# Kernel optimization log

Hardware: AMD Instinct MI355X
Metric: run time of the kernel (lower is better)

Reference implementation:

```python
import jax, jax.numpy as jnp
import numpy as np

BETA = 10.0  # fixed buffer: torch.ones(1, num_centers) * 10


def setup_inputs() -> dict:
    key = jax.random.key(0)
    k1, k2, k3 = jax.random.split(key, 3)
    n, M, d, n_out = 65536, 1024, 64, 3
    x = jax.random.normal(k1, (n, d), dtype=jnp.float32)
    centers = jax.random.normal(k2, (M, d), dtype=jnp.float32)
    # nn.Linear init in the module: weight ~ N(0, 0.02), bias = 0
    W = jax.random.normal(k3, (n_out, M + d), dtype=jnp.float32) * 0.02
    b = jnp.zeros((n_out,), dtype=jnp.float32)
    return {"x": x, "centers": centers, "W": W, "b": b}


def reference(x, centers, W, b):
    x2 = jnp.sum(x * x, axis=1, keepdims=True)          # [n, 1]
    c2 = jnp.sum(centers * centers, axis=1)             # [M]
    d2 = x2 + c2[None, :] - 2.0 * (x @ centers.T)       # [n, M]
    rbf = jnp.exp(-BETA * d2)                           # Gaussian RBF
    feat = jnp.concatenate([x, rbf], axis=1)            # [n, d + M]
    return feat @ W.T + b                               # [n, n_out]
```

## Files before the change

kernel.cpp:

```cpp
#include <hip/hip_runtime.h>
#include <math.h>

typedef short bf16x8 __attribute__((ext_vector_type(8)));
typedef float f32x4 __attribute__((ext_vector_type(4)));
typedef unsigned int uint32;

#define BETA 10.0f
#define THRESH -80.0f

#define C_OFF    0
#define C2_OFF   131072
#define XB_OFF   135168
#define W_OFF    151552
#define X2_OFF   152320
#define RED_OFF  152832
#define LDS_TOT  155904

__device__ __forceinline__ uint32 f2bf_rtne(float f) {
    uint32 u = __float_as_uint(f);
    u += 0x7FFFu + ((u >> 16) & 1u);
    return u >> 16;
}
__device__ __forceinline__ uint32 pk_rtne(float a, float b) {
    return f2bf_rtne(a) | (f2bf_rtne(b) << 16);
}
__device__ __forceinline__ float bf2f(short s) {
    return __uint_as_float(((uint32)(unsigned short)s) << 16);
}
__device__ __forceinline__ f32x4 vmax4(f32x4 a, f32x4 b) {
    f32x4 r;
    r[0] = fmaxf(a[0], b[0]); r[1] = fmaxf(a[1], b[1]);
    r[2] = fmaxf(a[2], b[2]); r[3] = fmaxf(a[3], b[3]);
    return r;
}

#define GLDS(g, l) __builtin_amdgcn_global_load_lds( \
    (const __attribute__((address_space(1))) unsigned int*)(g), \
    (__attribute__((address_space(3))) unsigned int*)(l), 16, 0, 0)

__global__ void rbfn_prep(const float* __restrict__ centers,
                          uint32* __restrict__ cbf,
                          float* __restrict__ c2m) {
    const int tid = threadIdx.x;
    const int j = blockIdx.x * 64 + (tid >> 2);
    const int seg = tid & 3;
    const float4* cp = (const float4*)(centers + j * 64 + seg * 16);
    const float4 f0 = cp[0], f1 = cp[1], f2 = cp[2], f3 = cp[3];
    float s = f0.x*f0.x + f0.y*f0.y + f0.z*f0.z + f0.w*f0.w
            + f1.x*f1.x + f1.y*f1.y + f1.z*f1.z + f1.w*f1.w
            + f2.x*f2.x + f2.y*f2.y + f2.z*f2.z + f2.w*f2.w
            + f3.x*f3.x + f3.y*f3.y + f3.z*f3.z + f3.w*f3.w;
    uint4 p0, p1;
    p0.x = pk_rtne(f0.x, f0.y); p0.y = pk_rtne(f0.z, f0.w);
    p0.z = pk_rtne(f1.x, f1.y); p0.w = pk_rtne(f1.z, f1.w);
    p1.x = pk_rtne(f2.x, f2.y); p1.y = pk_rtne(f2.z, f2.w);
    p1.z = pk_rtne(f3.x, f3.y); p1.w = pk_rtne(f3.z, f3.w);
    char* base = (char*)cbf + (j >> 4) * 2048 + (j & 15) * 16;
    *(uint4*)(base + (seg * 2 + 0) * 256) = p0;
    *(uint4*)(base + (seg * 2 + 1) * 256) = p1;
    s += __shfl_xor(s, 1);
    s += __shfl_xor(s, 2);
    if (seg == 0) c2m[j] = -BETA * s;
}

__global__ __launch_bounds__(512, 2) void rbfn_main(
    const float* __restrict__ x,
    const char* __restrict__ ws,
    const float* __restrict__ W,
    const float* __restrict__ bias,
    const float* __restrict__ centers,
    float* __restrict__ out)
{
    __shared__ __align__(16) char lds[LDS_TOT];

    const int tid = threadIdx.x;
    const int wv = tid >> 6;
    const int lane = tid & 63;
    const int quad = lane >> 4;
    const int l15 = lane & 15;
    const int row0 = blockIdx.x * 256;

    const float bb0 = bias[0], bb1 = bias[1], bb2 = bias[2];

    {
        const char* g = ws + wv * 1024 + lane * 16;
        char* l = lds + wv * 1024;
        #pragma unroll
        for (int it = 0; it < 16; ++it)
            GLDS(g + it * 8192, l + it * 8192);
        if (wv < 4)
            GLDS(ws + 131072 + wv * 1024 + lane * 16, lds + 131072 + wv * 1024);
    }

    float4 xv[2][4];
    {
        const float4* xg = (const float4*)(x + (size_t)row0 * 64);
        #pragma unroll
        for (int i = 0; i < 4; ++i) xv[0][i] = xg[tid + 512 * i];
        #pragma unroll
        for (int i = 0; i < 4; ++i) xv[1][i] = xg[2048 + tid + 512 * i];
    }
    if (tid < 48) {
        const int k = tid >> 4, c = tid & 15;
        *((float4*)(lds + W_OFF) + tid) = *((const float4*)(W + k * 1088) + c);
    }
    #pragma unroll
    for (int i = 0; i < 4; ++i) {
        const int f = tid + 512 * i;
        const float4 v = xv[0][i];
        const int row = f >> 4, sg = f & 15;
        uint2 q; q.x = pk_rtne(v.x, v.y); q.y = pk_rtne(v.z, v.w);
        *(uint2*)(lds + XB_OFF + (row >> 4) * 2048 + (sg >> 1) * 256 +
                  (row & 15) * 16 + (sg & 1) * 8) = q;
    }

    __syncthreads();

    bf16x8 af[8][2];
    const char* cB = lds + wv * 16384 + quad * 256 + l15 * 16;
    const float* c2p = (const float*)(lds + C2_OFF) + wv * 128 + l15;

    #pragma unroll
    for (int t = 0; t < 2; ++t) {
        #pragma unroll
        for (int rt = 0; rt < 8; ++rt) {
            const char* ab = lds + XB_OFF + rt * 2048 + l15 * 16;
            af[rt][0] = *(const bf16x8*)(ab + quad * 256);
            af[rt][1] = *(const bf16x8*)(ab + (4 + quad) * 256);
        }
        {
            const int r = tid >> 2, qq = tid & 3;
            const char* xr = lds + XB_OFF + (r >> 4) * 2048 + (r & 15) * 16;
            const bf16x8 h0 = *(const bf16x8*)(xr + (qq * 2 + 0) * 256);
            const bf16x8 h1 = *(const bf16x8*)(xr + (qq * 2 + 1) * 256);
            const float* w0 = (const float*)(lds + W_OFF) + 0 * 64 + qq * 16;
            const float* w1 = (const float*)(lds + W_OFF) + 1 * 64 + qq * 16;
            const float* w2 = (const float*)(lds + W_OFF) + 2 * 64 + qq * 16;
            float s2 = 0.f, d0 = 0.f, d1 = 0.f, d2 = 0.f;
            #pragma unroll
            for (int e = 0; e < 8; ++e) {
                const float a = bf2f(h0[e]), b = bf2f(h1[e]);
                s2 = fmaf(a, a, s2); s2 = fmaf(b, b, s2);
                d0 = fmaf(a, w0[e], d0); d0 = fmaf(b, w0[8 + e], d0);
                d1 = fmaf(a, w1[e], d1); d1 = fmaf(b, w1[8 + e], d1);
                d2 = fmaf(a, w2[e], d2); d2 = fmaf(b, w2[8 + e], d2);
            }
            #pragma unroll
            for (int m = 1; m <= 2; m <<= 1) {
                s2 += __shfl_xor(s2, m);
                d0 += __shfl_xor(d0, m);
                d1 += __shfl_xor(d1, m);
                d2 += __shfl_xor(d2, m);
            }
            if (qq == 0) {
                ((float*)(lds + X2_OFF))[r] = s2;
                float* red = (float*)(lds + RED_OFF + t * 1536);
                red[r * 3 + 0] = d0 + bb0;
                red[r * 3 + 1] = d1 + bb1;
                red[r * 3 + 2] = d2 + bb2;
            }
        }
        __syncthreads();

        if (t == 0) {
            #pragma unroll
            for (int i = 0; i < 4; ++i) {
                const int f = tid + 512 * i;
                const float4 v = xv[1][i];
                const int row = f >> 4, sg = f & 15;
                uint2 q; q.x = pk_rtne(v.x, v.y); q.y = pk_rtne(v.z, v.w);
                *(uint2*)(lds + XB_OFF + (row >> 4) * 2048 + (sg >> 1) * 256 +
                          (row & 15) * 16 + (sg & 1) * 8) = q;
            }
        }

        const float* px2 = (const float*)(lds + X2_OFF);
        float mn = 1e30f;
        #pragma unroll
        for (int rt = 0; rt < 8; ++rt) {
            const float4 q4 = *(const float4*)(px2 + rt * 16 + quad * 4);
            mn = fminf(mn, fminf(fminf(q4.x, q4.y), fminf(q4.z, q4.w)));
        }
        const float prermax = -BETA * mn;

        float gm = -1e30f;
        #pragma unroll
        for (int ct = 0; ct < 8; ++ct) {
            const bf16x8 b0 = *(const bf16x8*)(cB + ct * 2048);
            const bf16x8 b1 = *(const bf16x8*)(cB + ct * 2048 + 1024);
            const float c2v = c2p[ct * 16];
            f32x4 acc[8];
            #pragma unroll
            for (int rt = 0; rt < 8; ++rt) {
                const f32x4 z = {0.f, 0.f, 0.f, 0.f};
                acc[rt] = __builtin_amdgcn_mfma_f32_16x16x32_bf16(af[rt][0], b0, z, 0, 0, 0);
                acc[rt] = __builtin_amdgcn_mfma_f32_16x16x32_bf16(af[rt][1], b1, acc[rt], 0, 0, 0);
            }
            f32x4 m0 = vmax4(vmax4(acc[0], acc[1]), vmax4(acc[2], acc[3]));
            f32x4 m1 = vmax4(vmax4(acc[4], acc[5]), vmax4(acc[6], acc[7]));
            m0 = vmax4(m0, m1);
            const float m = fmaxf(fmaxf(m0[0], m0[1]), fmaxf(m0[2], m0[3]));
            gm = fmaxf(gm, fmaf(2.0f * BETA, m, c2v));
        }
        const float bound = gm + prermax;

        if (__builtin_expect(__ballot(bound > THRESH) != 0ull, 0)) {
            float* red = (float*)(lds + RED_OFF + t * 1536);
            #pragma clang loop unroll(disable)
            for (int ct = 0; ct < 8; ++ct) {
                const int j = wv * 128 + ct * 16 + l15;
                #pragma clang loop unroll(disable)
                for (int rr = 0; rr < 32; ++rr) {
                    const int r = (rr >> 2) * 16 + quad * 4 + (rr & 3);
                    const float* xr = x + (size_t)(row0 + t * 128 + r) * 64;
                    const float* cr = centers + (size_t)j * 64;
                    float d2 = 0.f;
                    #pragma clang loop unroll(disable)
                    for (int k = 0; k < 64; ++k) {
                        const float df = xr[k] - cr[k];
                        d2 = fmaf(df, df, d2);
                    }
                    const float arg = -BETA * d2;
                    if (arg > -87.f) {
                        const float e = expf(arg);
                        atomicAdd(&red[r * 3 + 0], e * W[0 * 1088 + 64 + j]);
                        atomicAdd(&red[r * 3 + 1], e * W[1 * 1088 + 64 + j]);
                        atomicAdd(&red[r * 3 + 2], e * W[2 * 1088 + 64 + j]);
                    }
                }
            }
        }
        __syncthreads();

        if (tid < 96)
            ((float4*)out)[blockIdx.x * 192 + t * 96 + tid] =
                *((const float4*)(lds + RED_OFF + t * 1536) + tid);
    }
}

extern "C" void kernel_launch(void* const* d_in, const int* in_sizes, int n_in,
                              void* d_out, int out_size, void* d_ws, size_t ws_size,
                              hipStream_t stream) {
    const float* x       = (const float*)d_in[0];
    const float* centers = (const float*)d_in[1];
    const float* W       = (const float*)d_in[2];
    const float* b       = (const float*)d_in[3];
    float* out = (float*)d_out;

    uint32* cbf = (uint32*)d_ws;
    float*  c2m = (float*)((char*)d_ws + 131072);

    const int n = in_sizes[0] / 64;

    rbfn_prep<<<16, 256, 0, stream>>>(centers, cbf, c2m);
    rbfn_main<<<n / 256, 512, 0, stream>>>(x, (const char*)d_ws, W, b, centers, out);
}
```

Before: 79.32 us.

## Split block work across 16 waves by row and column groups

Doubles the block to 1024 threads and splits the work: each wave now handles half the rows (rowgrp) of a 128-column slab (colgrp), so per-wave MFMA and register work halves. The x-norm and bias dot products are computed with 8 threads per row instead of 4, and the x2 buffer is double-buffered per tile. c2 values are hoisted into registers. The aim is more waves per CU to hide LDS and MFMA latency. In exchange the A fragments are loaded by more waves, and with about 153KB of LDS per block only one block fits per CU.

```diff
diff --git a/kernel.cpp b/kernel.cpp
--- a/kernel.cpp
+++ b/kernel.cpp
@@ -13,8 +13,8 @@
 #define XB_OFF   135168
 #define W_OFF    151552
 #define X2_OFF   152320
-#define RED_OFF  152832
-#define LDS_TOT  155904
+#define RED_OFF  153344
+#define LDS_TOT  156416
 
 __device__ __forceinline__ uint32 f2bf_rtne(float f) {
     uint32 u = __float_as_uint(f);
@@ -63,7 +63,7 @@
     if (seg == 0) c2m[j] = -BETA * s;
 }
 
-__global__ __launch_bounds__(512, 2) void rbfn_main(
+__global__ __launch_bounds__(1024) void rbfn_main(
     const float* __restrict__ x,
     const char* __restrict__ ws,
     const float* __restrict__ W,
@@ -78,35 +78,38 @@
     const int lane = tid & 63;
     const int quad = lane >> 4;
     const int l15 = lane & 15;
+    const int rowgrp = wv & 1;
+    const int colgrp = wv >> 1;
     const int row0 = blockIdx.x * 256;
 
     const float bb0 = bias[0], bb1 = bias[1], bb2 = bias[2];
 
     {
-        const char* g = ws + wv * 1024 + lane * 16;
-        char* l = lds + wv * 1024;
-        #pragma unroll
-        for (int it = 0; it < 16; ++it)
-            GLDS(g + it * 8192, l + it * 8192);
+        const char* g = ws + wv * 8192 + lane * 16;
+        char* l = lds + wv * 8192;
+        #pragma unroll
+        for (int it = 0; it < 8; ++it)
+            GLDS(g + it * 1024, l + it * 1024);
         if (wv < 4)
-            GLDS(ws + 131072 + wv * 1024 + lane * 16, lds + 131072 + wv * 1024);
-    }
-
-    float4 xv[2][4];
+            GLDS(ws + 131072 + wv * 1024 + lane * 16, lds + C2_OFF + wv * 1024);
+    }
+
+    float4 xv[2][2];
     {
         const float4* xg = (const float4*)(x + (size_t)row0 * 64);
         #pragma unroll
-        for (int i = 0; i < 4; ++i) xv[0][i] = xg[tid + 512 * i];
-        #pragma unroll
-        for (int i = 0; i < 4; ++i) xv[1][i] = xg[2048 + tid + 512 * i];
+        for (int t = 0; t < 2; ++t)
+            #pragma unroll
+            for (int i = 0; i < 2; ++i)
+                xv[t][i] = xg[t * 2048 + i * 1024 + tid];
     }
     if (tid < 48) {
         const int k = tid >> 4, c = tid & 15;
         *((float4*)(lds + W_OFF) + tid) = *((const float4*)(W + k * 1088) + c);
     }
     #pragma unroll
-    for (int i = 0; i < 4; ++i) {
-        const int f = tid + 512 * i;
+    for (int i = 0; i < 2; ++i) {
+        const int f = i * 1024 + tid;
         const float4 v = xv[0][i];
         const int row = f >> 4, sg = f & 15;
         uint2 q; q.x = pk_rtne(v.x, v.y); q.y = pk_rtne(v.z, v.w);
@@ -116,44 +119,48 @@
 
     __syncthreads();
 
-    bf16x8 af[8][2];
-    const char* cB = lds + wv * 16384 + quad * 256 + l15 * 16;
-    const float* c2p = (const float*)(lds + C2_OFF) + wv * 128 + l15;
+    float c2r[8];
+    {
+        const float* c2p = (const float*)(lds + C2_OFF) + colgrp * 128 + l15;
+        #pragma unroll
+        for (int ct = 0; ct < 8; ++ct) c2r[ct] = c2p[ct * 16];
+    }
+    const char* cB = lds + C_OFF + colgrp * 16384 + quad * 256 + l15 * 16;
 
     #pragma unroll
     for (int t = 0; t < 2; ++t) {
-        #pragma unroll
-        for (int rt = 0; rt < 8; ++rt) {
-            const char* ab = lds + XB_OFF + rt * 2048 + l15 * 16;
+        bf16x8 af[4][2];
+        #pragma unroll
+        for (int rt = 0; rt < 4; ++rt) {
+            const char* ab = lds + XB_OFF + (rowgrp * 4 + rt) * 2048 + l15 * 16;
             af[rt][0] = *(const bf16x8*)(ab + quad * 256);
             af[rt][1] = *(const bf16x8*)(ab + (4 + quad) * 256);
         }
         {
-            const int r = tid >> 2, qq = tid & 3;
-            const char* xr = lds + XB_OFF + (r >> 4) * 2048 + (r & 15) * 16;
-            const bf16x8 h0 = *(const bf16x8*)(xr + (qq * 2 + 0) * 256);
-            const bf16x8 h1 = *(const bf16x8*)(xr + (qq * 2 + 1) * 256);
-            const float* w0 = (const float*)(lds + W_OFF) + 0 * 64 + qq * 16;
-            const float* w1 = (const float*)(lds + W_OFF) + 1 * 64 + qq * 16;
-            const float* w2 = (const float*)(lds + W_OFF) + 2 * 64 + qq * 16;
+            const int r = tid >> 3, e = tid & 7;
+            const bf16x8 h = *(const bf16x8*)(lds + XB_OFF + (r >> 4) * 2048 +
+                                              e * 256 + (r & 15) * 16);
+            const float* w0 = (const float*)(lds + W_OFF) + 0 * 64 + e * 8;
+            const float* w1 = (const float*)(lds + W_OFF) + 1 * 64 + e * 8;
+            const float* w2 = (const float*)(lds + W_OFF) + 2 * 64 + e * 8;
             float s2 = 0.f, d0 = 0.f, d1 = 0.f, d2 = 0.f;
             #pragma unroll
-            for (int e = 0; e < 8; ++e) {
-                const float a = bf2f(h0[e]), b = bf2f(h1[e]);
-                s2 = fmaf(a, a, s2); s2 = fmaf(b, b, s2);
-                d0 = fmaf(a, w0[e], d0); d0 = fmaf(b, w0[8 + e], d0);
-                d1 = fmaf(a, w1[e], d1); d1 = fmaf(b, w1[8 + e], d1);
-                d2 = fmaf(a, w2[e], d2); d2 = fmaf(b, w2[8 + e], d2);
-            }
-            #pragma unroll
-            for (int m = 1; m <= 2; m <<= 1) {
+            for (int i = 0; i < 8; ++i) {
+                const float a = bf2f(h[i]);
+                s2 = fmaf(a, a, s2);
+                d0 = fmaf(a, w0[i], d0);
+                d1 = fmaf(a, w1[i], d1);
+                d2 = fmaf(a, w2[i], d2);
+            }
+            #pragma unroll
+            for (int m = 1; m <= 4; m <<= 1) {
                 s2 += __shfl_xor(s2, m);
                 d0 += __shfl_xor(d0, m);
                 d1 += __shfl_xor(d1, m);
                 d2 += __shfl_xor(d2, m);
             }
-            if (qq == 0) {
-                ((float*)(lds + X2_OFF))[r] = s2;
+            if (e == 0) {
+                ((float*)(lds + X2_OFF + t * 512))[r] = s2;
                 float* red = (float*)(lds + RED_OFF + t * 1536);
                 red[r * 3 + 0] = d0 + bb0;
                 red[r * 3 + 1] = d1 + bb1;
@@ -164,8 +171,8 @@
 
         if (t == 0) {
             #pragma unroll
-            for (int i = 0; i < 4; ++i) {
-                const int f = tid + 512 * i;
+            for (int i = 0; i < 2; ++i) {
+                const int f = i * 1024 + tid;
                 const float4 v = xv[1][i];
                 const int row = f >> 4, sg = f & 15;
                 uint2 q; q.x = pk_rtne(v.x, v.y); q.y = pk_rtne(v.z, v.w);
@@ -174,10 +181,10 @@
             }
         }
 
-        const float* px2 = (const float*)(lds + X2_OFF);
+        const float* px2 = (const float*)(lds + X2_OFF + t * 512) + rowgrp * 64;
         float mn = 1e30f;
         #pragma unroll
-        for (int rt = 0; rt < 8; ++rt) {
+        for (int rt = 0; rt < 4; ++rt) {
             const float4 q4 = *(const float4*)(px2 + rt * 16 + quad * 4);
             mn = fminf(mn, fminf(fminf(q4.x, q4.y), fminf(q4.z, q4.w)));
         }
@@ -188,19 +195,16 @@
         for (int ct = 0; ct < 8; ++ct) {
             const bf16x8 b0 = *(const bf16x8*)(cB + ct * 2048);
             const bf16x8 b1 = *(const bf16x8*)(cB + ct * 2048 + 1024);
-            const float c2v = c2p[ct * 16];
-            f32x4 acc[8];
-            #pragma unroll
-            for (int rt = 0; rt < 8; ++rt) {
+            f32x4 acc[4];
+            #pragma unroll
+            for (int rt = 0; rt < 4; ++rt) {
                 const f32x4 z = {0.f, 0.f, 0.f, 0.f};
                 acc[rt] = __builtin_amdgcn_mfma_f32_16x16x32_bf16(af[rt][0], b0, z, 0, 0, 0);
                 acc[rt] = __builtin_amdgcn_mfma_f32_16x16x32_bf16(af[rt][1], b1, acc[rt], 0, 0, 0);
             }
             f32x4 m0 = vmax4(vmax4(acc[0], acc[1]), vmax4(acc[2], acc[3]));
-            f32x4 m1 = vmax4(vmax4(acc[4], acc[5]), vmax4(acc[6], acc[7]));
-            m0 = vmax4(m0, m1);
             const float m = fmaxf(fmaxf(m0[0], m0[1]), fmaxf(m0[2], m0[3]));
-            gm = fmaxf(gm, fmaf(2.0f * BETA, m, c2v));
+            gm = fmaxf(gm, fmaf(2.0f * BETA, m, c2r[ct]));
         }
         const float bound = gm + prermax;
 
@@ -208,10 +212,10 @@
             float* red = (float*)(lds + RED_OFF + t * 1536);
             #pragma clang loop unroll(disable)
             for (int ct = 0; ct < 8; ++ct) {
-                const int j = wv * 128 + ct * 16 + l15;
+                const int j = colgrp * 128 + ct * 16 + l15;
                 #pragma clang loop unroll(disable)
-                for (int rr = 0; rr < 32; ++rr) {
-                    const int r = (rr >> 2) * 16 + quad * 4 + (rr & 3);
+                for (int rr = 0; rr < 16; ++rr) {
+                    const int r = rowgrp * 64 + (rr >> 2) * 16 + quad * 4 + (rr & 3);
                     const float* xr = x + (size_t)(row0 + t * 128 + r) * 64;
                     const float* cr = centers + (size_t)j * 64;
                     float d2 = 0.f;
@@ -253,5 +257,5 @@
     const int n = in_sizes[0] / 64;
 
     rbfn_prep<<<16, 256, 0, stream>>>(centers, cbf, c2m);
-    rbfn_main<<<n / 256, 512, 0, stream>>>(x, (const char*)d_ws, W, b, centers, out);
-}
+    rbfn_main<<<n / 256, 1024, 0, stream>>>(x, (const char*)d_ws, W, b, centers, out);
+}
```

New measurement: 81.53 us. +2.8%, slower.

## Fuse center prep into main kernel and compute norms and linear head via MFMA

Applied to the files above, without the earlier changes.

Removes the separate prep kernel. Each block now loads the fp32 centers, converts them to bf16 and swizzles them into LDS itself. The squared norms of x and centers come from MFMA self-products plus shuffles, and the x·W head uses a split hi/lo bf16 MFMA on wave 0, replacing the scalar LDS-based dot products. This saves a kernel launch and its dependency. In exchange, all 256 blocks redundantly convert the full center table, and norms are now taken from bf16-rounded inputs.

```diff
diff --git a/kernel.cpp b/kernel.cpp
--- a/kernel.cpp
+++ b/kernel.cpp
@@ -8,13 +8,10 @@
 #define BETA 10.0f
 #define THRESH -80.0f
 
-#define C_OFF    0
-#define C2_OFF   131072
-#define XB_OFF   135168
-#define W_OFF    151552
-#define X2_OFF   152320
-#define RED_OFF  152832
-#define LDS_TOT  155904
+#define C_OFF   0
+#define XB_OFF  131072
+#define RED_OFF 147456
+#define LDS_TOT 150528
 
 __device__ __forceinline__ uint32 f2bf_rtne(float f) {
     uint32 u = __float_as_uint(f);
@@ -23,9 +20,6 @@
 }
 __device__ __forceinline__ uint32 pk_rtne(float a, float b) {
     return f2bf_rtne(a) | (f2bf_rtne(b) << 16);
-}
-__device__ __forceinline__ float bf2f(short s) {
-    return __uint_as_float(((uint32)(unsigned short)s) << 16);
 }
 __device__ __forceinline__ f32x4 vmax4(f32x4 a, f32x4 b) {
     f32x4 r;
@@ -33,42 +27,13 @@
     r[2] = fmaxf(a[2], b[2]); r[3] = fmaxf(a[3], b[3]);
     return r;
 }
-
-#define GLDS(g, l) __builtin_amdgcn_global_load_lds( \
-    (const __attribute__((address_space(1))) unsigned int*)(g), \
-    (__attribute__((address_space(3))) unsigned int*)(l), 16, 0, 0)
-
-__global__ void rbfn_prep(const float* __restrict__ centers,
-                          uint32* __restrict__ cbf,
-                          float* __restrict__ c2m) {
-    const int tid = threadIdx.x;
-    const int j = blockIdx.x * 64 + (tid >> 2);
-    const int seg = tid & 3;
-    const float4* cp = (const float4*)(centers + j * 64 + seg * 16);
-    const float4 f0 = cp[0], f1 = cp[1], f2 = cp[2], f3 = cp[3];
-    float s = f0.x*f0.x + f0.y*f0.y + f0.z*f0.z + f0.w*f0.w
-            + f1.x*f1.x + f1.y*f1.y + f1.z*f1.z + f1.w*f1.w
-            + f2.x*f2.x + f2.y*f2.y + f2.z*f2.z + f2.w*f2.w
-            + f3.x*f3.x + f3.y*f3.y + f3.z*f3.z + f3.w*f3.w;
-    uint4 p0, p1;
-    p0.x = pk_rtne(f0.x, f0.y); p0.y = pk_rtne(f0.z, f0.w);
-    p0.z = pk_rtne(f1.x, f1.y); p0.w = pk_rtne(f1.z, f1.w);
-    p1.x = pk_rtne(f2.x, f2.y); p1.y = pk_rtne(f2.z, f2.w);
-    p1.z = pk_rtne(f3.x, f3.y); p1.w = pk_rtne(f3.z, f3.w);
-    char* base = (char*)cbf + (j >> 4) * 2048 + (j & 15) * 16;
-    *(uint4*)(base + (seg * 2 + 0) * 256) = p0;
-    *(uint4*)(base + (seg * 2 + 1) * 256) = p1;
-    s += __shfl_xor(s, 1);
-    s += __shfl_xor(s, 2);
-    if (seg == 0) c2m[j] = -BETA * s;
-}
-
-__global__ __launch_bounds__(512, 2) void rbfn_main(
+#define MFMA __builtin_amdgcn_mfma_f32_16x16x32_bf16
+
+__global__ __launch_bounds__(512) void rbfn_fused(
     const float* __restrict__ x,
-    const char* __restrict__ ws,
+    const float* __restrict__ centers,
     const float* __restrict__ W,
     const float* __restrict__ bias,
-    const float* __restrict__ centers,
     float* __restrict__ out)
 {
     __shared__ __align__(16) char lds[LDS_TOT];
@@ -80,127 +45,144 @@
     const int l15 = lane & 15;
     const int row0 = blockIdx.x * 256;
 
-    const float bb0 = bias[0], bb1 = bias[1], bb2 = bias[2];
-
-    {
-        const char* g = ws + wv * 1024 + lane * 16;
-        char* l = lds + wv * 1024;
-        #pragma unroll
-        for (int it = 0; it < 16; ++it)
-            GLDS(g + it * 8192, l + it * 8192);
-        if (wv < 4)
-            GLDS(ws + 131072 + wv * 1024 + lane * 16, lds + 131072 + wv * 1024);
-    }
-
-    float4 xv[2][4];
+    float4 x0[4], x1[4];
     {
         const float4* xg = (const float4*)(x + (size_t)row0 * 64);
         #pragma unroll
-        for (int i = 0; i < 4; ++i) xv[0][i] = xg[tid + 512 * i];
-        #pragma unroll
-        for (int i = 0; i < 4; ++i) xv[1][i] = xg[2048 + tid + 512 * i];
-    }
-    if (tid < 48) {
-        const int k = tid >> 4, c = tid & 15;
-        *((float4*)(lds + W_OFF) + tid) = *((const float4*)(W + k * 1088) + c);
+        for (int i = 0; i < 4; ++i) x0[i] = xg[i * 512 + tid];
+        #pragma unroll
+        for (int i = 0; i < 4; ++i) x1[i] = xg[2048 + i * 512 + tid];
+    }
+
+    {
+        const float4* cf4 = (const float4*)centers;
+        #pragma unroll 8
+        for (int i = 0; i < 32; ++i) {
+            const int f = i * 512 + tid;
+            const float4 v = cf4[f];
+            const int j = f >> 4, sg = f & 15;
+            uint2 q; q.x = pk_rtne(v.x, v.y); q.y = pk_rtne(v.z, v.w);
+            *(uint2*)(lds + C_OFF + (j >> 4) * 2048 + (sg >> 1) * 256 +
+                      (j & 15) * 16 + (sg & 1) * 8) = q;
+        }
     }
     #pragma unroll
     for (int i = 0; i < 4; ++i) {
-        const int f = tid + 512 * i;
-        const float4 v = xv[0][i];
-        const int row = f >> 4, sg = f & 15;
+        const int f = i * 512 + tid;
+        const float4 v = x0[i];
+        const int r = f >> 4, sg = f & 15;
         uint2 q; q.x = pk_rtne(v.x, v.y); q.y = pk_rtne(v.z, v.w);
-        *(uint2*)(lds + XB_OFF + (row >> 4) * 2048 + (sg >> 1) * 256 +
-                  (row & 15) * 16 + (sg & 1) * 8) = q;
+        *(uint2*)(lds + XB_OFF + (r >> 4) * 2048 + (sg >> 1) * 256 +
+                  (r & 15) * 16 + (sg & 1) * 8) = q;
+    }
+
+    bf16x8 bwh[2], bwl[2];
+    float bl = 0.f;
+    if (wv == 0) {
+        if (l15 < 3) bl = bias[l15];
+        #pragma unroll
+        for (int kk = 0; kk < 2; ++kk) {
+            bf16x8 h, l;
+            #pragma unroll
+            for (int e = 0; e < 8; ++e) {
+                const float w = (l15 < 3) ? W[l15 * 1088 + kk * 32 + quad * 8 + e] : 0.f;
+                const uint32 hb = f2bf_rtne(w);
+                h[e] = (short)hb;
+                l[e] = (short)f2bf_rtne(w - __uint_as_float(hb << 16));
+            }
+            bwh[kk] = h; bwl[kk] = l;
+        }
     }
 
     __syncthreads();
 
-    bf16x8 af[8][2];
-    const char* cB = lds + wv * 16384 + quad * 256 + l15 * 16;
-    const float* c2p = (const float*)(lds + C2_OFF) + wv * 128 + l15;
+    const char* cB = lds + C_OFF + wv * 16384 + quad * 256 + l15 * 16;
+    float c2r[8];
 
     #pragma unroll
     for (int t = 0; t < 2; ++t) {
+        bf16x8 af[8][2];
         #pragma unroll
         for (int rt = 0; rt < 8; ++rt) {
             const char* ab = lds + XB_OFF + rt * 2048 + l15 * 16;
             af[rt][0] = *(const bf16x8*)(ab + quad * 256);
             af[rt][1] = *(const bf16x8*)(ab + (4 + quad) * 256);
         }
-        {
-            const int r = tid >> 2, qq = tid & 3;
-            const char* xr = lds + XB_OFF + (r >> 4) * 2048 + (r & 15) * 16;
-            const bf16x8 h0 = *(const bf16x8*)(xr + (qq * 2 + 0) * 256);
-            const bf16x8 h1 = *(const bf16x8*)(xr + (qq * 2 + 1) * 256);
-            const float* w0 = (const float*)(lds + W_OFF) + 0 * 64 + qq * 16;
-            const float* w1 = (const float*)(lds + W_OFF) + 1 * 64 + qq * 16;
-            const float* w2 = (const float*)(lds + W_OFF) + 2 * 64 + qq * 16;
-            float s2 = 0.f, d0 = 0.f, d1 = 0.f, d2 = 0.f;
-            #pragma unroll
-            for (int e = 0; e < 8; ++e) {
-                const float a = bf2f(h0[e]), b = bf2f(h1[e]);
-                s2 = fmaf(a, a, s2); s2 = fmaf(b, b, s2);
-                d0 = fmaf(a, w0[e], d0); d0 = fmaf(b, w0[8 + e], d0);
-                d1 = fmaf(a, w1[e], d1); d1 = fmaf(b, w1[8 + e], d1);
-                d2 = fmaf(a, w2[e], d2); d2 = fmaf(b, w2[8 + e], d2);
-            }
-            #pragma unroll
-            for (int m = 1; m <= 2; m <<= 1) {
-                s2 += __shfl_xor(s2, m);
-                d0 += __shfl_xor(d0, m);
-                d1 += __shfl_xor(d1, m);
-                d2 += __shfl_xor(d2, m);
-            }
-            if (qq == 0) {
-                ((float*)(lds + X2_OFF))[r] = s2;
-                float* red = (float*)(lds + RED_OFF + t * 1536);
-                red[r * 3 + 0] = d0 + bb0;
-                red[r * 3 + 1] = d1 + bb1;
-                red[r * 3 + 2] = d2 + bb2;
-            }
-        }
+
+        float mn = 1e30f;
+        #pragma unroll
+        for (int rt = 0; rt < 8; ++rt) {
+            const f32x4 z = {0.f, 0.f, 0.f, 0.f};
+            f32x4 d = MFMA(af[rt][0], af[rt][0], z, 0, 0, 0);
+            d = MFMA(af[rt][1], af[rt][1], d, 0, 0, 0);
+            #pragma unroll
+            for (int reg = 0; reg < 4; ++reg)
+                mn = fminf(mn, __shfl(d[reg], quad * 20 + reg));
+        }
+        const float prermax = -BETA * mn;
+
+        if (t == 0) {
+            #pragma unroll
+            for (int ct = 0; ct < 8; ++ct) {
+                const bf16x8 b0 = *(const bf16x8*)(cB + ct * 2048);
+                const bf16x8 b1 = *(const bf16x8*)(cB + ct * 2048 + 1024);
+                const f32x4 z = {0.f, 0.f, 0.f, 0.f};
+                f32x4 d = MFMA(b0, b0, z, 0, 0, 0);
+                d = MFMA(b1, b1, d, 0, 0, 0);
+                const float dv = (l15 & 2) ? ((l15 & 1) ? d[3] : d[2])
+                                           : ((l15 & 1) ? d[1] : d[0]);
+                c2r[ct] = -BETA * __shfl(dv, (l15 >> 2) * 16 + l15);
+            }
+        }
+
+        if (wv == 0) {
+            float* redf = (float*)(lds + RED_OFF + t * 1536);
+            #pragma unroll
+            for (int rt = 0; rt < 8; ++rt) {
+                const f32x4 z = {0.f, 0.f, 0.f, 0.f};
+                f32x4 aw = MFMA(af[rt][0], bwh[0], z, 0, 0, 0);
+                aw = MFMA(af[rt][1], bwh[1], aw, 0, 0, 0);
+                aw = MFMA(af[rt][0], bwl[0], aw, 0, 0, 0);
+                aw = MFMA(af[rt][1], bwl[1], aw, 0, 0, 0);
+                if (l15 < 3) {
+                    #pragma unroll
+                    for (int reg = 0; reg < 4; ++reg)
+                        redf[(rt * 16 + quad * 4 + reg) * 3 + l15] = aw[reg] + bl;
+                }
+            }
+        }
+
         __syncthreads();
 
         if (t == 0) {
             #pragma unroll
             for (int i = 0; i < 4; ++i) {
-                const int f = tid + 512 * i;
-                const float4 v = xv[1][i];
-                const int row = f >> 4, sg = f & 15;
+                const int f = i * 512 + tid;
+                const float4 v = x1[i];
+                const int r = f >> 4, sg = f & 15;
                 uint2 q; q.x = pk_rtne(v.x, v.y); q.y = pk_rtne(v.z, v.w);
-                *(uint2*)(lds + XB_OFF + (row >> 4) * 2048 + (sg >> 1) * 256 +
-                          (row & 15) * 16 + (sg & 1) * 8) = q;
-            }
-        }
-
-        const float* px2 = (const float*)(lds + X2_OFF);
-        float mn = 1e30f;
-        #pragma unroll
-        for (int rt = 0; rt < 8; ++rt) {
-            const float4 q4 = *(const float4*)(px2 + rt * 16 + quad * 4);
-            mn = fminf(mn, fminf(fminf(q4.x, q4.y), fminf(q4.z, q4.w)));
-        }
-        const float prermax = -BETA * mn;
+                *(uint2*)(lds + XB_OFF + (r >> 4) * 2048 + (sg >> 1) * 256 +
+                          (r & 15) * 16 + (sg & 1) * 8) = q;
+            }
+        }
 
         float gm = -1e30f;
         #pragma unroll
         for (int ct = 0; ct < 8; ++ct) {
             const bf16x8 b0 = *(const bf16x8*)(cB + ct * 2048);
             const bf16x8 b1 = *(const bf16x8*)(cB + ct * 2048 + 1024);
-            const float c2v = c2p[ct * 16];
             f32x4 acc[8];
             #pragma unroll
             for (int rt = 0; rt < 8; ++rt) {
                 const f32x4 z = {0.f, 0.f, 0.f, 0.f};
-                acc[rt] = __builtin_amdgcn_mfma_f32_16x16x32_bf16(af[rt][0], b0, z, 0, 0, 0);
-                acc[rt] = __builtin_amdgcn_mfma_f32_16x16x32_bf16(af[rt][1], b1, acc[rt], 0, 0, 0);
+                acc[rt] = MFMA(af[rt][0], b0, z, 0, 0, 0);
+                acc[rt] = MFMA(af[rt][1], b1, acc[rt], 0, 0, 0);
             }
             f32x4 m0 = vmax4(vmax4(acc[0], acc[1]), vmax4(acc[2], acc[3]));
             f32x4 m1 = vmax4(vmax4(acc[4], acc[5]), vmax4(acc[6], acc[7]));
             m0 = vmax4(m0, m1);
             const float m = fmaxf(fmaxf(m0[0], m0[1]), fmaxf(m0[2], m0[3]));
-            gm = fmaxf(gm, fmaf(2.0f * BETA, m, c2v));
+            gm = fmaxf(gm, fmaf(2.0f * BETA, m, c2r[ct]));
         }
         const float bound = gm + prermax;
 
@@ -247,11 +229,6 @@
     const float* b       = (const float*)d_in[3];
     float* out = (float*)d_out;
 
-    uint32* cbf = (uint32*)d_ws;
-    float*  c2m = (float*)((char*)d_ws + 131072);
-
     const int n = in_sizes[0] / 64;
-
-    rbfn_prep<<<16, 256, 0, stream>>>(centers, cbf, c2m);
-    rbfn_main<<<n / 256, 512, 0, stream>>>(x, (const char*)d_ws, W, b, centers, out);
-}
+    rbfn_fused<<<n / 256, 512, 0, stream>>>(x, centers, W, b, out);
+}
```

Result: slower. 81.51 us (+2.8%).
